# Kernel optimization log

Measured on AMD Instinct MI355X. Metric: run time of the kernel, lower is better.

## Reference

```python
import jax, jax.numpy as jnp
import numpy as np

N, C, H, W = 1, 128, 512, 512
CH = C // 2  # channels seen by each 1x1 conv


def setup_inputs() -> dict:
    key = jax.random.key(0)
    ks = jax.random.split(key, 6)
    return {
        "lst": jax.random.normal(ks[0], (N, C, H, W), dtype=jnp.float32),
        "gui": jax.random.normal(ks[1], (N, C, H, W), dtype=jnp.float32),
        "w1": jax.random.normal(ks[2], (CH, CH), dtype=jnp.float32) * 0.05,  # conv1 weight (out,in) of 1x1 kernel
        "b1": jax.random.normal(ks[3], (CH,), dtype=jnp.float32) * 0.05,
        "w2": jax.random.normal(ks[4], (CH, CH), dtype=jnp.float32) * 0.05,  # conv2 weight
        "b2": jax.random.normal(ks[5], (CH,), dtype=jnp.float32) * 0.05,
        "p": 2,
    }


def _conv1x1(x, w, b):
    # x: [N, CH, H, W]; 1x1 conv == per-pixel channel mixing GEMM
    return jnp.einsum('oc,nchw->nohw', w, x) + b[None, :, None, None]


def reference(lst, gui, w1, b1, w2, b2, p):
    # channel_mask = arange(C) % p == 0 selects channels 0, p, 2p, ... -> strided slice [:, ::p]
    # Exchanged channels: out_lst gets conv2(gui_masked), out_gui gets conv1(lst_masked).
    # Unmasked channels pass through unchanged (out initialized as copy of input).
    out_lst = lst.at[:, ::p].set(_conv1x1(gui[:, ::p], w2, b2))
    out_gui = gui.at[:, ::p].set(_conv1x1(lst[:, ::p], w1, b1))
    return (out_lst, out_gui)
```

## Files before the change

kernel.cpp:

```cpp
#include <hip/hip_runtime.h>

#define HW (512 * 512)
#define NC 128
#define CH 64

__global__ __launch_bounds__(256) void conv_even_kernel(
    const float* __restrict__ lst, const float* __restrict__ gui,
    const float* __restrict__ w1, const float* __restrict__ b1,
    const float* __restrict__ w2, const float* __restrict__ b2,
    float* __restrict__ out_lst, float* __restrict__ out_gui)
{
    const int pix = blockIdx.x * 256 + threadIdx.x;

    float x[CH];

    #pragma unroll
    for (int c = 0; c < CH; ++c) x[c] = gui[(2 * c) * HW + pix];

    for (int k = 0; k < CH; ++k) {
        float acc = b2[k];
        #pragma unroll
        for (int c = 0; c < CH; ++c) acc = fmaf(w2[k * CH + c], x[c], acc);
        out_lst[(2 * k) * HW + pix] = acc;
    }

    #pragma unroll
    for (int c = 0; c < CH; ++c) x[c] = lst[(2 * c) * HW + pix];

    for (int k = 0; k < CH; ++k) {
        float acc = b1[k];
        #pragma unroll
        for (int c = 0; c < CH; ++c) acc = fmaf(w1[k * CH + c], x[c], acc);
        out_gui[(2 * k) * HW + pix] = acc;
    }
}

__global__ __launch_bounds__(256) void copy_odd_kernel(
    const float4* __restrict__ lst, const float4* __restrict__ gui,
    float4* __restrict__ out_lst, float4* __restrict__ out_gui)
{
    const int i = blockIdx.x * 256 + threadIdx.x;
    const int c = i >> 16;
    const int j = i & 0xFFFF;
    const int off = ((2 * c + 1) << 16) + j;

    out_lst[off] = lst[off];
    out_gui[off] = gui[off];
}

extern "C" void kernel_launch(void* const* d_in, const int* in_sizes, int n_in,
                              void* d_out, int out_size, void* d_ws, size_t ws_size,
                              hipStream_t stream) {
    const float* lst = (const float*)d_in[0];
    const float* gui = (const float*)d_in[1];
    const float* w1  = (const float*)d_in[2];
    const float* b1  = (const float*)d_in[3];
    const float* w2  = (const float*)d_in[4];
    const float* b2  = (const float*)d_in[5];

    float* out_lst = (float*)d_out;
    float* out_gui = out_lst + (size_t)NC * HW;

    conv_even_kernel<<<HW / 256, 256, 0, stream>>>(lst, gui, w1, b1, w2, b2,
                                                   out_lst, out_gui);

    copy_odd_kernel<<<(64 * (HW / 4)) / 256, 256, 0, stream>>>(
        (const float4*)lst, (const float4*)gui, (float4*)out_lst, (float4*)out_gui);
}
```

Before: 627.6 us.

## Fuse conv and odd-channel copy into one launch with register-blocked accumulation

Merges the 1x1 conv kernel and the odd-channel passthrough copy into a single heterogeneous grid: the first blocks do the convolution, the rest do the copy with 4 float4 elements per thread. The conv loop is reorganized to keep 64 output accumulators in registers and stream inputs in chunks of 8 channels, instead of holding all 64 inputs and reducing one output at a time. This is meant to remove a kernel launch boundary, let the copy overlap with the conv, and improve memory-level parallelism. The 64-float accumulator array raises register pressure, which may reduce occupancy.

```diff
diff --git a/kernel.cpp b/kernel.cpp
--- a/kernel.cpp
+++ b/kernel.cpp
@@ -1,51 +1,99 @@
 #include <hip/hip_runtime.h>
 
 #define HW (512 * 512)
-#define NC 128
 #define CH 64
+#define CONV_BLOCKS 1024
+#define COPY_BLOCKS 4096
+#define COPY_THREADS (COPY_BLOCKS * 256)
+#define COPY_R 4
 
-__global__ __launch_bounds__(256) void conv_even_kernel(
+__global__ __launch_bounds__(256) void fused_exchange_kernel(
     const float* __restrict__ lst, const float* __restrict__ gui,
     const float* __restrict__ w1, const float* __restrict__ b1,
     const float* __restrict__ w2, const float* __restrict__ b2,
     float* __restrict__ out_lst, float* __restrict__ out_gui)
 {
-    const int pix = blockIdx.x * 256 + threadIdx.x;
+    const int b = blockIdx.x;
 
-    float x[CH];
+    if (b < CONV_BLOCKS) {
+        const int pix = b * 256 + threadIdx.x;
 
-    #pragma unroll
-    for (int c = 0; c < CH; ++c) x[c] = gui[(2 * c) * HW + pix];
+        {
+            float acc[CH];
+            #pragma unroll
+            for (int k = 0; k < CH; ++k) acc[k] = b2[k];
 
-    for (int k = 0; k < CH; ++k) {
-        float acc = b2[k];
+            for (int cc = 0; cc < CH; cc += 8) {
+                float x[8];
+                #pragma unroll
+                for (int j = 0; j < 8; ++j)
+                    x[j] = gui[(size_t)(2 * (cc + j)) * HW + pix];
+                #pragma unroll
+                for (int k = 0; k < CH; ++k) {
+                    const float* wr = w2 + k * CH + cc;
+                    float a = acc[k];
+                    a = fmaf(wr[0], x[0], a);
+                    a = fmaf(wr[1], x[1], a);
+                    a = fmaf(wr[2], x[2], a);
+                    a = fmaf(wr[3], x[3], a);
+                    a = fmaf(wr[4], x[4], a);
+                    a = fmaf(wr[5], x[5], a);
+                    a = fmaf(wr[6], x[6], a);
+                    a = fmaf(wr[7], x[7], a);
+                    acc[k] = a;
+                }
+            }
+            #pragma unroll
+            for (int k = 0; k < CH; ++k)
+                out_lst[(size_t)(2 * k) * HW + pix] = acc[k];
+        }
+
+        {
+            float acc[CH];
+            #pragma unroll
+            for (int k = 0; k < CH; ++k) acc[k] = b1[k];
+
+            for (int cc = 0; cc < CH; cc += 8) {
+                float x[8];
+                #pragma unroll
+                for (int j = 0; j < 8; ++j)
+                    x[j] = lst[(size_t)(2 * (cc + j)) * HW + pix];
+                #pragma unroll
+                for (int k = 0; k < CH; ++k) {
+                    const float* wr = w1 + k * CH + cc;
+                    float a = acc[k];
+                    a = fmaf(wr[0], x[0], a);
+                    a = fmaf(wr[1], x[1], a);
+                    a = fmaf(wr[2], x[2], a);
+                    a = fmaf(wr[3], x[3], a);
+                    a = fmaf(wr[4], x[4], a);
+                    a = fmaf(wr[5], x[5], a);
+                    a = fmaf(wr[6], x[6], a);
+                    a = fmaf(wr[7], x[7], a);
+                    acc[k] = a;
+                }
+            }
+            #pragma unroll
+            for (int k = 0; k < CH; ++k)
+                out_gui[(size_t)(2 * k) * HW + pix] = acc[k];
+        }
+    } else {
+        const int t = (b - CONV_BLOCKS) * 256 + threadIdx.x;
+        const float4* l4  = (const float4*)lst;
+        const float4* g4  = (const float4*)gui;
+        float4* ol4 = (float4*)out_lst;
+        float4* og4 = (float4*)out_gui;
+
         #pragma unroll
-        for (int c = 0; c < CH; ++c) acc = fmaf(w2[k * CH + c], x[c], acc);
-        out_lst[(2 * k) * HW + pix] = acc;
+        for (int r = 0; r < COPY_R; ++r) {
+            const int idx = t + r * COPY_THREADS;
+            const int c   = idx >> 16;
+            const int j   = idx & 0xFFFF;
+            const int off = ((2 * c + 1) << 16) + j;
+            ol4[off] = l4[off];
+            og4[off] = g4[off];
+        }
     }
-
-    #pragma unroll
-    for (int c = 0; c < CH; ++c) x[c] = lst[(2 * c) * HW + pix];
-
-    for (int k = 0; k < CH; ++k) {
-        float acc = b1[k];
-        #pragma unroll
-        for (int c = 0; c < CH; ++c) acc = fmaf(w1[k * CH + c], x[c], acc);
-        out_gui[(2 * k) * HW + pix] = acc;
-    }
-}
-
-__global__ __launch_bounds__(256) void copy_odd_kernel(
-    const float4* __restrict__ lst, const float4* __restrict__ gui,
-    float4* __restrict__ out_lst, float4* __restrict__ out_gui)
-{
-    const int i = blockIdx.x * 256 + threadIdx.x;
-    const int c = i >> 16;
-    const int j = i & 0xFFFF;
-    const int off = ((2 * c + 1) << 16) + j;
-
-    out_lst[off] = lst[off];
-    out_gui[off] = gui[off];
 }
 
 extern "C" void kernel_launch(void* const* d_in, const int* in_sizes, int n_in,
@@ -59,11 +107,8 @@
     const float* b2  = (const float*)d_in[5];
 
     float* out_lst = (float*)d_out;
-    float* out_gui = out_lst + (size_t)NC * HW;
+    float* out_gui = out_lst + (size_t)128 * HW;
 
-    conv_even_kernel<<<HW / 256, 256, 0, stream>>>(lst, gui, w1, b1, w2, b2,
-                                                   out_lst, out_gui);
-
-    copy_odd_kernel<<<(64 * (HW / 4)) / 256, 256, 0, stream>>>(
-        (const float4*)lst, (const float4*)gui, (float4*)out_lst, (float4*)out_gui);
+    fused_exchange_kernel<<<CONV_BLOCKS + COPY_BLOCKS, 256, 0, stream>>>(
+        lst, gui, w1, b1, w2, b2, out_lst, out_gui);
 }
```

Measured after the change: 552.6 us. 1.14x faster.
